# Kernel optimization log

Measured on AMD Instinct MI355X. Metric: run time of the kernel, lower is better.

Reference implementation:

```python
import jax, jax.numpy as jnp
import numpy as np

B, S, D, OUT = 4, 4096, 256, 64
SCALE = 1.0 / np.sqrt(64.0)  # module hard-codes / 64**0.5


def setup_inputs() -> dict:
    key = jax.random.key(0)
    k1, k2 = jax.random.split(key)
    x = jax.random.normal(k1, (B, S, D), dtype=jnp.float32)
    kernel = jax.random.normal(k2, (3, D, OUT), dtype=jnp.float32) * 0.05
    return {"x": x, "kernel": kernel}


def reference(x, kernel):
    # Single-head attention with shared-input Q/K/V projections.
    q = jnp.einsum('bsd,do->bso', x, kernel[0])
    k = jnp.einsum('bsd,do->bso', x, kernel[1])
    v = jnp.einsum('bsd,do->bso', x, kernel[2])
    scores = jnp.einsum('bqo,bko->bqk', q, k) * SCALE  # [B,S,S]
    attn = jax.nn.softmax(scores, axis=-1)
    return jnp.einsum('bqk,bko->bqo', attn, v)  # [B,S,OUT]
```

## Files before the change

### kernel.cpp

```cpp
#include <hip/hip_runtime.h>

#define SLEN 4096
#define NB 4
#define DIN 256
#define DOUT 64
#define KVSPLIT 4
#define KVBLK 64
#define QBLK 64
#define NT ((SLEN / KVSPLIT) / KVBLK)

typedef _Float16 f16;
typedef _Float16 f16x8 __attribute__((ext_vector_type(8)));
typedef _Float16 f16x4 __attribute__((ext_vector_type(4)));
typedef float f32x4 __attribute__((ext_vector_type(4)));

#define QSCALE 0.1803368801111204f
#define PSHIFT2 4.328085122666891f

#define GLD16(gsrc, ldst)                                          \
  __builtin_amdgcn_global_load_lds(                                \
      (const __attribute__((address_space(1))) void*)(gsrc),       \
      (__attribute__((address_space(3))) void*)(ldst), 16, 0, 0)

__global__ __launch_bounds__(256) void wt_kernel(
    const float* __restrict__ w, f16* __restrict__ wth) {
  for (int idx = blockIdx.x * 256 + threadIdx.x; idx < 3 * DIN * DOUT;
       idx += gridDim.x * 256) {
    int m = idx / (DIN * DOUT);
    int r = idx - m * (DIN * DOUT);
    int k = r >> 6, o = r & 63;
    wth[(m * DOUT + o) * DIN + k] = (f16)w[idx];
  }
}

__global__ __launch_bounds__(64) void proj_kernel(
    const float* __restrict__ x, const f16* __restrict__ wth,
    f16* __restrict__ qh, f16* __restrict__ kh, f16* __restrict__ vth) {
  __shared__ alignas(16) f16 tbuf[64 * 24];
  const int lane = threadIdx.x;
  const int c = lane & 15, g = lane >> 4;
  const int m = blockIdx.y;
  const int tb = blockIdx.x * 16;
  const int b = tb >> 12, s0 = tb & 4095;

  f16x8 a[8];
  {
    const float* xr = x + (size_t)(tb + c) * DIN + g * 8;
#pragma unroll
    for (int ks = 0; ks < 8; ++ks) {
      f32x4 lo = *(const f32x4*)(xr + ks * 32);
      f32x4 hi = *(const f32x4*)(xr + ks * 32 + 4);
      f16x8 av;
#pragma unroll
      for (int j = 0; j < 4; ++j) { av[j] = (f16)lo[j]; av[j + 4] = (f16)hi[j]; }
      a[ks] = av;
    }
  }

  const f16* wb = wth + (size_t)m * DOUT * DIN + (size_t)c * DIN + g * 8;
  f32x4 acc[4];
#pragma unroll
  for (int nt = 0; nt < 4; ++nt) acc[nt] = (f32x4){0.f, 0.f, 0.f, 0.f};
#pragma unroll
  for (int ks = 0; ks < 8; ++ks)
#pragma unroll
    for (int nt = 0; nt < 4; ++nt) {
      f16x8 bf = *(const f16x8*)(wb + (size_t)(nt * 16) * DIN + ks * 32);
      acc[nt] = __builtin_amdgcn_mfma_f32_16x16x32_f16(a[ks], bf, acc[nt], 0, 0, 0);
    }

  if (m < 2) {
#pragma unroll
    for (int nt = 0; nt < 4; ++nt)
#pragma unroll
      for (int rr = 0; rr < 4; ++rr)
        tbuf[(4 * g + rr) * 72 + nt * 16 + c] =
            (f16)(m == 0 ? acc[nt][rr] * QSCALE : acc[nt][rr]);
    const int rw = lane >> 2, cb = (lane & 3) * 16;
    f16x8 r0 = *(const f16x8*)&tbuf[rw * 72 + cb];
    f16x8 r1 = *(const f16x8*)&tbuf[rw * 72 + cb + 8];
    f16* dst = (m == 0 ? qh : kh) + (size_t)(tb + rw) * DOUT + cb;
    *(f16x8*)(dst) = r0;
    *(f16x8*)(dst + 8) = r1;
  } else {
#pragma unroll
    for (int nt = 0; nt < 4; ++nt)
#pragma unroll
      for (int rr = 0; rr < 4; ++rr)
        tbuf[(nt * 16 + c) * 24 + 4 * g + rr] = (f16)acc[nt][rr];
    f16x8 r0 = *(const f16x8*)&tbuf[lane * 24];
    f16x8 r1 = *(const f16x8*)&tbuf[lane * 24 + 8];
    f16* dst = vth + ((size_t)b * DOUT + lane) * SLEN + s0;
    *(f16x8*)(dst) = r0;
    *(f16x8*)(dst + 8) = r1;
  }
}

__global__ __launch_bounds__(256, 4) void attn_kernel(
    const f16* __restrict__ qh, const f16* __restrict__ kh,
    const f16* __restrict__ vth, float* __restrict__ out,
    float* __restrict__ pL) {
  __shared__ alignas(16) f16 kb[2][KVBLK * 64];
  __shared__ alignas(16) f16 vb[2][KVBLK * 64];
  __shared__ alignas(16) f16 pbuf[4][16 * 64];

  const int tid = threadIdx.x;
  const int lane = tid & 63;
  const int c = lane & 15, g = lane >> 4;
  const int wv = tid >> 6;

  const int wg = ((blockIdx.x & 7) << 7) + (blockIdx.x >> 3);
  const int b = wg >> 8;
  const int split = (wg >> 6) & 3;
  const int qb = wg & 63;
  const int q0 = qb * QBLK + wv * 16;
  const int kv0 = split * (SLEN / KVSPLIT);

  f16* plds = pbuf[wv];

  const int srow = tid >> 3;
  const int scol = (tid & 7) * 8;
  const f16* kgbase = kh + (size_t)b * SLEN * DOUT;
  const f16* vgbase = vth + (size_t)b * DOUT * SLEN;

  f16x8 qf[2];
  {
    const f16* qr = qh + ((size_t)(b * SLEN + q0 + c)) * DOUT + g * 8;
    qf[0] = *(const f16x8*)(qr);
    qf[1] = *(const f16x8*)(qr + 32);
  }

  f32x4 oacc[4];
#pragma unroll
  for (int nt = 0; nt < 4; ++nt) oacc[nt] = (f32x4){0.f, 0.f, 0.f, 0.f};
  float lrun = 0.f;

  auto stage = [&](int sel, int kv) {
#pragma unroll
    for (int rr = 0; rr < 2; ++rr) {
      int r = srow + rr * 32;
      int sw = scol ^ ((r & 7) << 3);
      GLD16(kgbase + (size_t)(kv + r) * DOUT + sw,
            (char*)(&kb[sel][0]) + wv * 1024 + rr * 4096);
      GLD16(vgbase + (size_t)r * SLEN + kv + sw,
            (char*)(&vb[sel][0]) + wv * 1024 + rr * 4096);
    }
  };

  stage(0, kv0);
  __syncthreads();

  for (int t = 0; t < NT; ++t) {
    const int sel = t & 1;
    if (t + 1 < NT) stage(sel ^ 1, kv0 + (t + 1) * KVBLK);

    f32x4 sacc[4];
    __builtin_amdgcn_s_setprio(1);
#pragma unroll
    for (int t4 = 0; t4 < 4; ++t4) {
      sacc[t4] = (f32x4){0.f, 0.f, 0.f, 0.f};
      f16x8 k0 = *(const f16x8*)&kb[sel][(16 * t4 + c) * 64 + 8 * (g ^ (c & 7))];
      f16x8 k1 = *(const f16x8*)&kb[sel][(16 * t4 + c) * 64 + 8 * ((g + 4) ^ (c & 7))];
      sacc[t4] = __builtin_amdgcn_mfma_f32_16x16x32_f16(k0, qf[0], sacc[t4], 0, 0, 0);
      sacc[t4] = __builtin_amdgcn_mfma_f32_16x16x32_f16(k1, qf[1], sacc[t4], 0, 0, 0);
    }
    __builtin_amdgcn_s_setprio(0);

    f16x4 pk[4];
#pragma unroll
    for (int t4 = 0; t4 < 4; ++t4)
#pragma unroll
      for (int r = 0; r < 4; ++r) {
        float p = exp2f(sacc[t4][r] - PSHIFT2);
        lrun += p;
        pk[t4][r] = (f16)p;
      }

#pragma unroll
    for (int t4 = 0; t4 < 4; ++t4)
      *(f16x4*)&plds[c * 64 + ((16 * t4 + 4 * g) ^ ((c & 7) << 3))] = pk[t4];

    __builtin_amdgcn_s_setprio(1);
#pragma unroll
    for (int s2 = 0; s2 < 2; ++s2) {
      f16x8 pa = *(const f16x8*)&plds[c * 64 + ((s2 * 32 + g * 8) ^ ((c & 7) << 3))];
#pragma unroll
      for (int nt = 0; nt < 4; ++nt) {
        f16x8 vf = *(const f16x8*)&vb[sel][(16 * nt + c) * 64 + 8 * ((g + 4 * s2) ^ (c & 7))];
        oacc[nt] = __builtin_amdgcn_mfma_f32_16x16x32_f16(pa, vf, oacc[nt], 0, 0, 0);
      }
    }
    __builtin_amdgcn_s_setprio(0);

    __syncthreads();
  }

  const size_t rowb = (size_t)b * SLEN + q0;
  float* po = out + rowb * DOUT;
#pragma unroll
  for (int nt = 0; nt < 4; ++nt)
#pragma unroll
    for (int r = 0; r < 4; ++r)
      atomicAdd(&po[(size_t)(4 * g + r) * DOUT + nt * 16 + c], oacc[nt][r]);
  lrun += __shfl_xor(lrun, 16);
  lrun += __shfl_xor(lrun, 32);
  if (lane < 16) atomicAdd(&pL[rowb + lane], lrun);
}

__global__ __launch_bounds__(256) void norm_kernel(
    float* __restrict__ out, const float* __restrict__ pL) {
  int i = blockIdx.x * 256 + threadIdx.x;
  int row = i >> 4;
  float rl = 1.0f / pL[row];
  f32x4 o = *(const f32x4*)&out[(size_t)i * 4];
  o *= rl;
  *(f32x4*)&out[(size_t)i * 4] = o;
}

extern "C" void kernel_launch(void* const* d_in, const int* in_sizes, int n_in,
                              void* d_out, int out_size, void* d_ws, size_t ws_size,
                              hipStream_t stream) {
  const float* x = (const float*)d_in[0];
  const float* w = (const float*)d_in[1];
  float* out = (float*)d_out;

  const size_t NE = (size_t)NB * SLEN * DOUT;
  f16* qh = (f16*)d_ws;
  f16* kh = qh + NE;
  f16* vth = kh + NE;
  f16* wth = vth + NE;
  float* pL = (float*)(wth + 3 * DIN * DOUT);

  hipMemsetAsync(out, 0, NE * sizeof(float), stream);
  hipMemsetAsync(pL, 0, (size_t)NB * SLEN * sizeof(float), stream);
  hipLaunchKernelGGL(wt_kernel, dim3(12), dim3(256), 0, stream, w, wth);
  hipLaunchKernelGGL(proj_kernel, dim3(NB * SLEN / 16, 3), dim3(64), 0, stream,
                     x, wth, qh, kh, vth);
  hipLaunchKernelGGL(attn_kernel, dim3(NB * KVSPLIT * (SLEN / QBLK)), dim3(256),
                     0, stream, qh, kh, vth, out, pL);
  hipLaunchKernelGGL(norm_kernel, dim3(NB * SLEN * DOUT / 4 / 256), dim3(256),
                     0, stream, out, pL);
}
```

Before: 130.7 us.

## Double query rows per wave in attention and fuse memsets into setup kernel

Each wave now processes 32 query rows instead of 16 (QBLK 128), so every K/V tile staged into LDS feeds twice as many MFMAs. This halves K/V global traffic and staging per query and adds independent MFMA chains to hide latency. The two hipMemsetAsync calls are folded into the weight-transpose kernel, which removes launch overhead. In exchange, register and LDS pressure rise (launch bounds lowered to 3), and the grid drops to 512 blocks, which may underfill the CUs.

```diff
diff --git a/kernel.cpp b/kernel.cpp
--- a/kernel.cpp
+++ b/kernel.cpp
@@ -6,7 +6,7 @@
 #define DOUT 64
 #define KVSPLIT 4
 #define KVBLK 64
-#define QBLK 64
+#define QBLK 128
 #define NT ((SLEN / KVSPLIT) / KVBLK)
 
 typedef _Float16 f16;
@@ -22,14 +22,20 @@
       (const __attribute__((address_space(1))) void*)(gsrc),       \
       (__attribute__((address_space(3))) void*)(ldst), 16, 0, 0)
 
-__global__ __launch_bounds__(256) void wt_kernel(
-    const float* __restrict__ w, f16* __restrict__ wth) {
-  for (int idx = blockIdx.x * 256 + threadIdx.x; idx < 3 * DIN * DOUT;
-       idx += gridDim.x * 256) {
-    int m = idx / (DIN * DOUT);
-    int r = idx - m * (DIN * DOUT);
+__global__ __launch_bounds__(256) void setup_kernel(
+    const float* __restrict__ w, f16* __restrict__ wth,
+    float* __restrict__ out, float* __restrict__ pL) {
+  int gtid = blockIdx.x * 256 + threadIdx.x;
+  if (gtid < 3 * DIN * DOUT) {
+    int m = gtid / (DIN * DOUT);
+    int r = gtid - m * (DIN * DOUT);
     int k = r >> 6, o = r & 63;
-    wth[(m * DOUT + o) * DIN + k] = (f16)w[idx];
+    wth[(m * DOUT + o) * DIN + k] = (f16)w[gtid];
+  }
+  const int ntot = NB * SLEN * DOUT;
+  for (int i = gtid; i < ntot + NB * SLEN; i += 65536) {
+    if (i < ntot) out[i] = 0.f;
+    else pL[i - ntot] = 0.f;
   }
 }
 
@@ -96,24 +102,24 @@
   }
 }
 
-__global__ __launch_bounds__(256, 4) void attn_kernel(
+__global__ __launch_bounds__(256, 3) void attn_kernel(
     const f16* __restrict__ qh, const f16* __restrict__ kh,
     const f16* __restrict__ vth, float* __restrict__ out,
     float* __restrict__ pL) {
   __shared__ alignas(16) f16 kb[2][KVBLK * 64];
   __shared__ alignas(16) f16 vb[2][KVBLK * 64];
-  __shared__ alignas(16) f16 pbuf[4][16 * 64];
+  __shared__ alignas(16) f16 pbuf[4][32 * 64];
 
   const int tid = threadIdx.x;
   const int lane = tid & 63;
   const int c = lane & 15, g = lane >> 4;
   const int wv = tid >> 6;
 
-  const int wg = ((blockIdx.x & 7) << 7) + (blockIdx.x >> 3);
-  const int b = wg >> 8;
-  const int split = (wg >> 6) & 3;
-  const int qb = wg & 63;
-  const int q0 = qb * QBLK + wv * 16;
+  const int wg = ((blockIdx.x & 7) << 6) + (blockIdx.x >> 3);
+  const int b = wg >> 7;
+  const int split = (wg >> 5) & 3;
+  const int qb = wg & 31;
+  const int q0 = qb * QBLK + wv * 32;
   const int kv0 = split * (SLEN / KVSPLIT);
 
   f16* plds = pbuf[wv];
@@ -123,17 +129,21 @@
   const f16* kgbase = kh + (size_t)b * SLEN * DOUT;
   const f16* vgbase = vth + (size_t)b * DOUT * SLEN;
 
-  f16x8 qf[2];
-  {
-    const f16* qr = qh + ((size_t)(b * SLEN + q0 + c)) * DOUT + g * 8;
-    qf[0] = *(const f16x8*)(qr);
-    qf[1] = *(const f16x8*)(qr + 32);
-  }
-
-  f32x4 oacc[4];
-#pragma unroll
-  for (int nt = 0; nt < 4; ++nt) oacc[nt] = (f32x4){0.f, 0.f, 0.f, 0.f};
-  float lrun = 0.f;
+  f16x8 qf[4];
+#pragma unroll
+  for (int h = 0; h < 2; ++h) {
+    const f16* qr = qh + ((size_t)(b * SLEN + q0 + 16 * h + c)) * DOUT + g * 8;
+    qf[2 * h] = *(const f16x8*)(qr);
+    qf[2 * h + 1] = *(const f16x8*)(qr + 32);
+  }
+
+  f32x4 o0[4], o1[4];
+#pragma unroll
+  for (int nt = 0; nt < 4; ++nt) {
+    o0[nt] = (f32x4){0.f, 0.f, 0.f, 0.f};
+    o1[nt] = (f32x4){0.f, 0.f, 0.f, 0.f};
+  }
+  float lr0 = 0.f, lr1 = 0.f;
 
   auto stage = [&](int sel, int kv) {
 #pragma unroll
@@ -154,40 +164,51 @@
     const int sel = t & 1;
     if (t + 1 < NT) stage(sel ^ 1, kv0 + (t + 1) * KVBLK);
 
-    f32x4 sacc[4];
+    f32x4 s0[4], s1[4];
     __builtin_amdgcn_s_setprio(1);
 #pragma unroll
     for (int t4 = 0; t4 < 4; ++t4) {
-      sacc[t4] = (f32x4){0.f, 0.f, 0.f, 0.f};
       f16x8 k0 = *(const f16x8*)&kb[sel][(16 * t4 + c) * 64 + 8 * (g ^ (c & 7))];
       f16x8 k1 = *(const f16x8*)&kb[sel][(16 * t4 + c) * 64 + 8 * ((g + 4) ^ (c & 7))];
-      sacc[t4] = __builtin_amdgcn_mfma_f32_16x16x32_f16(k0, qf[0], sacc[t4], 0, 0, 0);
-      sacc[t4] = __builtin_amdgcn_mfma_f32_16x16x32_f16(k1, qf[1], sacc[t4], 0, 0, 0);
+      f32x4 z = (f32x4){0.f, 0.f, 0.f, 0.f};
+      s0[t4] = __builtin_amdgcn_mfma_f32_16x16x32_f16(k0, qf[0], z, 0, 0, 0);
+      s0[t4] = __builtin_amdgcn_mfma_f32_16x16x32_f16(k1, qf[1], s0[t4], 0, 0, 0);
+      s1[t4] = __builtin_amdgcn_mfma_f32_16x16x32_f16(k0, qf[2], z, 0, 0, 0);
+      s1[t4] = __builtin_amdgcn_mfma_f32_16x16x32_f16(k1, qf[3], s1[t4], 0, 0, 0);
     }
     __builtin_amdgcn_s_setprio(0);
 
-    f16x4 pk[4];
+    f16x4 pk0[4], pk1[4];
 #pragma unroll
     for (int t4 = 0; t4 < 4; ++t4)
 #pragma unroll
       for (int r = 0; r < 4; ++r) {
-        float p = exp2f(sacc[t4][r] - PSHIFT2);
-        lrun += p;
-        pk[t4][r] = (f16)p;
+        float p0 = exp2f(s0[t4][r] - PSHIFT2);
+        float p1 = exp2f(s1[t4][r] - PSHIFT2);
+        lr0 += p0;
+        lr1 += p1;
+        pk0[t4][r] = (f16)p0;
+        pk1[t4][r] = (f16)p1;
       }
 
 #pragma unroll
-    for (int t4 = 0; t4 < 4; ++t4)
-      *(f16x4*)&plds[c * 64 + ((16 * t4 + 4 * g) ^ ((c & 7) << 3))] = pk[t4];
+    for (int t4 = 0; t4 < 4; ++t4) {
+      int sw = (16 * t4 + 4 * g) ^ ((c & 7) << 3);
+      *(f16x4*)&plds[c * 64 + sw] = pk0[t4];
+      *(f16x4*)&plds[1024 + c * 64 + sw] = pk1[t4];
+    }
 
     __builtin_amdgcn_s_setprio(1);
 #pragma unroll
     for (int s2 = 0; s2 < 2; ++s2) {
-      f16x8 pa = *(const f16x8*)&plds[c * 64 + ((s2 * 32 + g * 8) ^ ((c & 7) << 3))];
+      int sw = (s2 * 32 + g * 8) ^ ((c & 7) << 3);
+      f16x8 pa0 = *(const f16x8*)&plds[c * 64 + sw];
+      f16x8 pa1 = *(const f16x8*)&plds[1024 + c * 64 + sw];
 #pragma unroll
       for (int nt = 0; nt < 4; ++nt) {
         f16x8 vf = *(const f16x8*)&vb[sel][(16 * nt + c) * 64 + 8 * ((g + 4 * s2) ^ (c & 7))];
-        oacc[nt] = __builtin_amdgcn_mfma_f32_16x16x32_f16(pa, vf, oacc[nt], 0, 0, 0);
+        o0[nt] = __builtin_amdgcn_mfma_f32_16x16x32_f16(pa0, vf, o0[nt], 0, 0, 0);
+        o1[nt] = __builtin_amdgcn_mfma_f32_16x16x32_f16(pa1, vf, o1[nt], 0, 0, 0);
       }
     }
     __builtin_amdgcn_s_setprio(0);
@@ -196,15 +217,21 @@
   }
 
   const size_t rowb = (size_t)b * SLEN + q0;
-  float* po = out + rowb * DOUT;
 #pragma unroll
   for (int nt = 0; nt < 4; ++nt)
 #pragma unroll
-    for (int r = 0; r < 4; ++r)
-      atomicAdd(&po[(size_t)(4 * g + r) * DOUT + nt * 16 + c], oacc[nt][r]);
-  lrun += __shfl_xor(lrun, 16);
-  lrun += __shfl_xor(lrun, 32);
-  if (lane < 16) atomicAdd(&pL[rowb + lane], lrun);
+    for (int r = 0; r < 4; ++r) {
+      atomicAdd(&out[(rowb + 4 * g + r) * DOUT + nt * 16 + c], o0[nt][r]);
+      atomicAdd(&out[(rowb + 16 + 4 * g + r) * DOUT + nt * 16 + c], o1[nt][r]);
+    }
+  lr0 += __shfl_xor(lr0, 16);
+  lr0 += __shfl_xor(lr0, 32);
+  lr1 += __shfl_xor(lr1, 16);
+  lr1 += __shfl_xor(lr1, 32);
+  if (lane < 16) {
+    atomicAdd(&pL[rowb + lane], lr0);
+    atomicAdd(&pL[rowb + 16 + lane], lr1);
+  }
 }
 
 __global__ __launch_bounds__(256) void norm_kernel(
@@ -231,9 +258,8 @@
   f16* wth = vth + NE;
   float* pL = (float*)(wth + 3 * DIN * DOUT);
 
-  hipMemsetAsync(out, 0, NE * sizeof(float), stream);
-  hipMemsetAsync(pL, 0, (size_t)NB * SLEN * sizeof(float), stream);
-  hipLaunchKernelGGL(wt_kernel, dim3(12), dim3(256), 0, stream, w, wth);
+  hipLaunchKernelGGL(setup_kernel, dim3(256), dim3(256), 0, stream,
+                     w, wth, out, pL);
   hipLaunchKernelGGL(proj_kernel, dim3(NB * SLEN / 16, 3), dim3(64), 0, stream,
                      x, wth, qh, kh, vth);
   hipLaunchKernelGGL(attn_kernel, dim3(NB * KVSPLIT * (SLEN / QBLK)), dim3(256),
```

Measured after the change: 127.6 us. 2.4% less time.

## Double query block per workgroup, replace atomics with split partials and combine kernel

Applied to the files above, without the earlier changes.

Raises the query block to 128 rows with 512-thread workgroups, so each K/V tile staged in LDS serves twice as many query rows and each thread issues one async load per tile. The per-split partial outputs and row sums are now written to workspace buffers and reduced in a combine kernel, which removes the two memsets and the atomic adds. The exp shift is folded into the MFMA accumulator init, conversion uses packed round-toward-zero, and the weight-transpose kernel is simplified. In exchange the workspace traffic grows by four partial output arrays, and the grid has half as many, larger workgroups.

```diff
diff --git a/kernel.cpp b/kernel.cpp
--- a/kernel.cpp
+++ b/kernel.cpp
@@ -6,30 +6,36 @@
 #define DOUT 64
 #define KVSPLIT 4
 #define KVBLK 64
-#define QBLK 64
-#define NT ((SLEN / KVSPLIT) / KVBLK)
+#define QBLK 128
+#define CHUNK (SLEN / KVSPLIT)
+#define NT (CHUNK / KVBLK)
 
 typedef _Float16 f16;
 typedef _Float16 f16x8 __attribute__((ext_vector_type(8)));
 typedef _Float16 f16x4 __attribute__((ext_vector_type(4)));
+typedef _Float16 f16x2 __attribute__((ext_vector_type(2)));
 typedef float f32x4 __attribute__((ext_vector_type(4)));
 
 #define QSCALE 0.1803368801111204f
 #define PSHIFT2 4.328085122666891f
+
+static __device__ __forceinline__ f16x2 pkrtz(float a, float b) {
+  return __builtin_bit_cast(f16x2, __builtin_amdgcn_cvt_pkrtz(a, b));
+}
 
 #define GLD16(gsrc, ldst)                                          \
   __builtin_amdgcn_global_load_lds(                                \
       (const __attribute__((address_space(1))) void*)(gsrc),       \
       (__attribute__((address_space(3))) void*)(ldst), 16, 0, 0)
 
-__global__ __launch_bounds__(256) void wt_kernel(
+__global__ __launch_bounds__(256) void setup_kernel(
     const float* __restrict__ w, f16* __restrict__ wth) {
-  for (int idx = blockIdx.x * 256 + threadIdx.x; idx < 3 * DIN * DOUT;
-       idx += gridDim.x * 256) {
-    int m = idx / (DIN * DOUT);
-    int r = idx - m * (DIN * DOUT);
+  int gtid = blockIdx.x * 256 + threadIdx.x;
+  if (gtid < 3 * DIN * DOUT) {
+    int m = gtid / (DIN * DOUT);
+    int r = gtid - m * (DIN * DOUT);
     int k = r >> 6, o = r & 63;
-    wth[(m * DOUT + o) * DIN + k] = (f16)w[idx];
+    wth[(m * DOUT + o) * DIN + k] = (f16)w[gtid];
   }
 }
 
@@ -96,25 +102,25 @@
   }
 }
 
-__global__ __launch_bounds__(256, 4) void attn_kernel(
+__global__ __launch_bounds__(512, 4) void attn_kernel(
     const f16* __restrict__ qh, const f16* __restrict__ kh,
-    const f16* __restrict__ vth, float* __restrict__ out,
+    const f16* __restrict__ vth, float* __restrict__ pO,
     float* __restrict__ pL) {
   __shared__ alignas(16) f16 kb[2][KVBLK * 64];
   __shared__ alignas(16) f16 vb[2][KVBLK * 64];
-  __shared__ alignas(16) f16 pbuf[4][16 * 64];
+  __shared__ alignas(16) f16 pbuf[8][16 * 64];
 
   const int tid = threadIdx.x;
   const int lane = tid & 63;
   const int c = lane & 15, g = lane >> 4;
   const int wv = tid >> 6;
 
-  const int wg = ((blockIdx.x & 7) << 7) + (blockIdx.x >> 3);
-  const int b = wg >> 8;
-  const int split = (wg >> 6) & 3;
-  const int qb = wg & 63;
+  const int wg = ((blockIdx.x & 7) << 6) + (blockIdx.x >> 3);
+  const int b = wg >> 7;
+  const int split = (wg >> 5) & 3;
+  const int qb = wg & 31;
   const int q0 = qb * QBLK + wv * 16;
-  const int kv0 = split * (SLEN / KVSPLIT);
+  const int kv0 = split * CHUNK;
 
   f16* plds = pbuf[wv];
 
@@ -134,22 +140,20 @@
 #pragma unroll
   for (int nt = 0; nt < 4; ++nt) oacc[nt] = (f32x4){0.f, 0.f, 0.f, 0.f};
   float lrun = 0.f;
+  const f32x4 zinit = (f32x4){-PSHIFT2, -PSHIFT2, -PSHIFT2, -PSHIFT2};
 
   auto stage = [&](int sel, int kv) {
-#pragma unroll
-    for (int rr = 0; rr < 2; ++rr) {
-      int r = srow + rr * 32;
-      int sw = scol ^ ((r & 7) << 3);
-      GLD16(kgbase + (size_t)(kv + r) * DOUT + sw,
-            (char*)(&kb[sel][0]) + wv * 1024 + rr * 4096);
-      GLD16(vgbase + (size_t)r * SLEN + kv + sw,
-            (char*)(&vb[sel][0]) + wv * 1024 + rr * 4096);
-    }
+    int sw = scol ^ ((srow & 7) << 3);
+    GLD16(kgbase + (size_t)(kv + srow) * DOUT + sw,
+          (char*)(&kb[sel][0]) + wv * 1024);
+    GLD16(vgbase + (size_t)srow * SLEN + kv + sw,
+          (char*)(&vb[sel][0]) + wv * 1024);
   };
 
   stage(0, kv0);
   __syncthreads();
 
+#pragma unroll 2
   for (int t = 0; t < NT; ++t) {
     const int sel = t & 1;
     if (t + 1 < NT) stage(sel ^ 1, kv0 + (t + 1) * KVBLK);
@@ -158,23 +162,22 @@
     __builtin_amdgcn_s_setprio(1);
 #pragma unroll
     for (int t4 = 0; t4 < 4; ++t4) {
-      sacc[t4] = (f32x4){0.f, 0.f, 0.f, 0.f};
       f16x8 k0 = *(const f16x8*)&kb[sel][(16 * t4 + c) * 64 + 8 * (g ^ (c & 7))];
       f16x8 k1 = *(const f16x8*)&kb[sel][(16 * t4 + c) * 64 + 8 * ((g + 4) ^ (c & 7))];
-      sacc[t4] = __builtin_amdgcn_mfma_f32_16x16x32_f16(k0, qf[0], sacc[t4], 0, 0, 0);
+      sacc[t4] = __builtin_amdgcn_mfma_f32_16x16x32_f16(k0, qf[0], zinit, 0, 0, 0);
       sacc[t4] = __builtin_amdgcn_mfma_f32_16x16x32_f16(k1, qf[1], sacc[t4], 0, 0, 0);
     }
     __builtin_amdgcn_s_setprio(0);
 
     f16x4 pk[4];
 #pragma unroll
-    for (int t4 = 0; t4 < 4; ++t4)
-#pragma unroll
-      for (int r = 0; r < 4; ++r) {
-        float p = exp2f(sacc[t4][r] - PSHIFT2);
-        lrun += p;
-        pk[t4][r] = (f16)p;
-      }
+    for (int t4 = 0; t4 < 4; ++t4) {
+      float e0 = exp2f(sacc[t4][0]), e1 = exp2f(sacc[t4][1]);
+      float e2 = exp2f(sacc[t4][2]), e3 = exp2f(sacc[t4][3]);
+      lrun += (e0 + e1) + (e2 + e3);
+      f16x2 a0 = pkrtz(e0, e1), a1 = pkrtz(e2, e3);
+      pk[t4] = (f16x4){a0[0], a0[1], a1[0], a1[1]};
+    }
 
 #pragma unroll
     for (int t4 = 0; t4 < 4; ++t4)
@@ -196,25 +199,32 @@
   }
 
   const size_t rowb = (size_t)b * SLEN + q0;
-  float* po = out + rowb * DOUT;
+  float* po = pO + ((size_t)split * (NB * SLEN) + rowb) * DOUT;
 #pragma unroll
   for (int nt = 0; nt < 4; ++nt)
 #pragma unroll
     for (int r = 0; r < 4; ++r)
-      atomicAdd(&po[(size_t)(4 * g + r) * DOUT + nt * 16 + c], oacc[nt][r]);
+      po[(size_t)(4 * g + r) * DOUT + nt * 16 + c] = oacc[nt][r];
   lrun += __shfl_xor(lrun, 16);
   lrun += __shfl_xor(lrun, 32);
-  if (lane < 16) atomicAdd(&pL[rowb + lane], lrun);
-}
-
-__global__ __launch_bounds__(256) void norm_kernel(
-    float* __restrict__ out, const float* __restrict__ pL) {
+  if (lane < 16) pL[(size_t)split * (NB * SLEN) + rowb + lane] = lrun;
+}
+
+__global__ __launch_bounds__(256) void combine_kernel(
+    const float* __restrict__ pO, const float* __restrict__ pL,
+    float* __restrict__ out) {
   int i = blockIdx.x * 256 + threadIdx.x;
   int row = i >> 4;
-  float rl = 1.0f / pL[row];
-  f32x4 o = *(const f32x4*)&out[(size_t)i * 4];
-  o *= rl;
-  *(f32x4*)&out[(size_t)i * 4] = o;
+  int c4 = (i & 15) * 4;
+  f32x4 a = (f32x4){0.f, 0.f, 0.f, 0.f};
+  float L = 0.f;
+#pragma unroll
+  for (int s = 0; s < KVSPLIT; ++s) {
+    a += *(const f32x4*)&pO[((size_t)s * (NB * SLEN) + row) * DOUT + c4];
+    L += pL[(size_t)s * (NB * SLEN) + row];
+  }
+  float rl = 1.0f / L;
+  *(f32x4*)&out[(size_t)row * DOUT + c4] = a * rl;
 }
 
 extern "C" void kernel_launch(void* const* d_in, const int* in_sizes, int n_in,
@@ -229,15 +239,14 @@
   f16* kh = qh + NE;
   f16* vth = kh + NE;
   f16* wth = vth + NE;
-  float* pL = (float*)(wth + 3 * DIN * DOUT);
-
-  hipMemsetAsync(out, 0, NE * sizeof(float), stream);
-  hipMemsetAsync(pL, 0, (size_t)NB * SLEN * sizeof(float), stream);
-  hipLaunchKernelGGL(wt_kernel, dim3(12), dim3(256), 0, stream, w, wth);
+  float* pO = (float*)(wth + 3 * DIN * DOUT);
+  float* pL = pO + (size_t)KVSPLIT * NE;
+
+  hipLaunchKernelGGL(setup_kernel, dim3(192), dim3(256), 0, stream, w, wth);
   hipLaunchKernelGGL(proj_kernel, dim3(NB * SLEN / 16, 3), dim3(64), 0, stream,
                      x, wth, qh, kh, vth);
-  hipLaunchKernelGGL(attn_kernel, dim3(NB * KVSPLIT * (SLEN / QBLK)), dim3(256),
-                     0, stream, qh, kh, vth, out, pL);
-  hipLaunchKernelGGL(norm_kernel, dim3(NB * SLEN * DOUT / 4 / 256), dim3(256),
-                     0, stream, out, pL);
-}
+  hipLaunchKernelGGL(attn_kernel, dim3(NB * KVSPLIT * (SLEN / QBLK)), dim3(512),
+                     0, stream, qh, kh, vth, pO, pL);
+  hipLaunchKernelGGL(combine_kernel, dim3(NB * SLEN * DOUT / 4 / 256), dim3(256),
+                     0, stream, pO, pL, out);
+}
```

After: 114.6 us. 1.14x faster.
